# Performance work log

Measured on AMD Instinct MI355X. Metric: run time of the kernel, lower is better.

## Reference

```python
import jax, jax.numpy as jnp
import numpy as np

N_SENS, N_HID, N_MOT = 10000, 400000, 1000
E_SH, E_HH, E_HM = 4_000_000, 16_000_000, 400_000
BETA, THR, SLOPE = 0.9, 1.0, 25.0  # snn.Leaky(beta, threshold), surrogate.fast_sigmoid(slope=25)

# Heaviside spike with fast-sigmoid surrogate gradient (matches snnTorch)
@jax.custom_vjp
def spike(x):
    return (x > 0).astype(x.dtype)

def _spike_fwd(x):
    return (x > 0).astype(x.dtype), x

def _spike_bwd(x, g):
    return (g / (SLOPE * jnp.abs(x) + 1.0) ** 2,)

spike.defvjp(_spike_fwd, _spike_bwd)

def lif(inp, mem):
    # snn.Leaky, reset_mechanism='zero': mem = beta*mem + I; spike; reset to 0 where spiked
    mem = BETA * mem + inp
    spk = spike(mem - THR)
    mem = mem - jax.lax.stop_gradient(spk) * mem  # reset detached, as in snnTorch
    return spk, mem

def spmm_t(pre_idx, post_idx, w, pre_spikes, n_post):
    # torch.sparse.mm(W^T, pre_spikes): gather pre activity along edges, scatter-add to post
    contrib = w * pre_spikes[pre_idx]          # [E]
    return jax.ops.segment_sum(contrib, post_idx, num_segments=n_post)

def setup_inputs() -> dict:
    key = jax.random.key(0)
    ks = jax.random.split(key, 16)
    std_sh = 1.0 / np.sqrt(N_SENS * 0.001)
    std_hh = 1.0 / np.sqrt(N_HID * 0.0001)
    std_hm = 1.0 / np.sqrt(N_HID * 0.001)
    return {
        "sensory_input": jax.random.uniform(ks[0], (N_SENS,), jnp.float32),
        "sensory_mem": jax.random.uniform(ks[1], (N_SENS,), jnp.float32),
        "hidden_mem": jax.random.uniform(ks[2], (N_HID,), jnp.float32),
        "motor_mem": jax.random.uniform(ks[3], (N_MOT,), jnp.float32),
        "hidden_prev_spikes": (jax.random.uniform(ks[4], (N_HID,)) < 0.05).astype(jnp.float32),
        "w_sh": jax.random.normal(ks[5], (E_SH,), jnp.float32) * std_sh,
        "w_hh": jax.random.normal(ks[6], (E_HH,), jnp.float32) * std_hh,
        "w_hm": jax.random.normal(ks[7], (E_HM,), jnp.float32) * std_hm,
        "sh_pre": jax.random.randint(ks[8], (E_SH,), 0, N_SENS, jnp.int32),
        "sh_post": jax.random.randint(ks[9], (E_SH,), 0, N_HID, jnp.int32),
        "hh_pre": jax.random.randint(ks[10], (E_HH,), 0, N_HID, jnp.int32),
        "hh_post": jax.random.randint(ks[11], (E_HH,), 0, N_HID, jnp.int32),
        "hm_pre": jax.random.randint(ks[12], (E_HM,), 0, N_HID, jnp.int32),
        "hm_post": jax.random.randint(ks[13], (E_HM,), 0, N_MOT, jnp.int32),
    }

def reference(sensory_input, sensory_mem, hidden_mem, motor_mem, hidden_prev_spikes,
              w_sh, w_hh, w_hm, sh_pre, sh_post, hh_pre, hh_post, hm_pre, hm_post):
    sens_spk, _ = lif(sensory_input * 5.0, sensory_mem)
    hid_in = spmm_t(sh_pre, sh_post, w_sh, sens_spk, N_HID)
    hid_in = hid_in + 0.5 * spmm_t(hh_pre, hh_post, w_hh, hidden_prev_spikes, N_HID)
    hid_spk, _ = lif(hid_in * 5.0, hidden_mem)
    mot_in = spmm_t(hm_pre, hm_post, w_hm, hid_spk, N_MOT)
    mot_spk, _ = lif(mot_in * 20.0, motor_mem)
    return mot_spk
```

## Files before the change

kernel.cpp:

```cpp
#include <hip/hip_runtime.h>


#define N_SENS 10000
#define N_HID  400000
#define N_MOT  1000

#define CHUNK_LOG 14
#define CHUNK     (1 << CHUNK_LOG)
#define NBUCKET   25
#define CAP       204800
#define NCOPY     10

#define SENS_MW   320
#define HID_MW    12512

#define BUF_SH    4096
#define BUF_HH    2048
#define EPT_SH    4
#define EPT_HH    16

#define NB_HM     64

__global__ void make_masks(const float* __restrict__ sens_in,
                           const float* __restrict__ sens_mem,
                           const float* __restrict__ hid_prev,
                           uint2* __restrict__ smask,
                           uint2* __restrict__ hmask, int nb_sens) {
    bool pred = false;
    int i;
    uint2* dst;
    int maxw;
    if ((int)blockIdx.x < nb_sens) {
        i = blockIdx.x * blockDim.x + threadIdx.x;
        if (i < N_SENS) pred = (0.9f * sens_mem[i] + 5.0f * sens_in[i]) > 1.0f;
        dst = smask; maxw = SENS_MW / 2;
    } else {
        i = (blockIdx.x - nb_sens) * blockDim.x + threadIdx.x;
        if (i < N_HID) pred = (hid_prev[i] != 0.0f);
        dst = hmask; maxw = HID_MW / 2;
    }
    unsigned long long b = __ballot(pred);
    if ((threadIdx.x & 63) == 0) {
        int w = i >> 6;
        if (w < maxw) dst[w] = make_uint2((unsigned)b, (unsigned)(b >> 32));
    }
}

template <int MW, int BUFCAP, int EPT>
__global__ __launch_bounds__(1024, 8)
void bin_onepass(const int* __restrict__ pre, const int* __restrict__ post,
                 const float* __restrict__ w, const unsigned* __restrict__ gmask,
                 int n_e, float scale,
                 uint2* __restrict__ pairs, int* __restrict__ gcursor,
                 float* __restrict__ extra) {
    __shared__ unsigned sm[MW];
    __shared__ uint2 buf[BUFCAP];
    __shared__ int h[4][32];
    __shared__ int gb[32];
    __shared__ int lcur[32];
    __shared__ int total;

    const int tid = threadIdx.x;
    const int lane = tid & 63;
    for (int i = tid; i < MW; i += 1024) sm[i] = gmask[i];
    if (tid < 128) ((int*)h)[tid] = 0;
    if (tid == 0) total = 0;
    __syncthreads();

    int blockStart = blockIdx.x * (1024 * EPT);
    #pragma unroll
    for (int j = 0; j < EPT; ++j) {
        int e = blockStart + j * 1024 + tid;
        bool act = false;
        unsigned p = 0; float wv = 0.0f;
        if (e < n_e) {
            int pr = pre[e];
            act = (sm[pr >> 5] >> (pr & 31)) & 1u;
            if (act) { p = (unsigned)post[e]; wv = scale * w[e]; }
        }
        unsigned long long m = __ballot(act);
        if (m) {
            int rank = __popcll(m & ((1ull << lane) - 1ull));
            int base = 0;
            if (lane == 0) base = atomicAdd(&total, __popcll(m));
            base = __shfl(base, 0);
            if (act) {
                int k = base + rank;
                if (k < BUFCAP) buf[k] = make_uint2(p, __float_as_uint(wv));
                else atomicAdd(&extra[p], wv);
            }
        }
    }
    __syncthreads();
    int tot = total; if (tot > BUFCAP) tot = BUFCAP;

    int rep = (tid >> 6) & 3;
    for (int k = tid; k < tot; k += 1024)
        atomicAdd(&h[rep][buf[k].x >> CHUNK_LOG], 1);
    __syncthreads();
    if (tid < NBUCKET) {
        int hb = h[0][tid] + h[1][tid] + h[2][tid] + h[3][tid];
        gb[tid] = hb ? atomicAdd(&gcursor[tid], hb) : 0;
        lcur[tid] = 0;
    }
    __syncthreads();

    for (int k = tid; k < tot; k += 1024) {
        uint2 u = buf[k];
        int b = u.x >> CHUNK_LOG;
        int s = atomicAdd(&lcur[b], 1);
        int pos = gb[b] + s;
        if (pos < CAP)
            pairs[(size_t)b * CAP + pos] =
                make_uint2(u.x & (CHUNK - 1), u.y);
        else
            atomicAdd(&extra[u.x], __uint_as_float(u.y));
    }
}

__global__ __launch_bounds__(1024, 8)
void accum_bucket(const uint2* __restrict__ pairs,
                  const int* __restrict__ cursors,
                  float* __restrict__ partials) {
    int bucket = blockIdx.x / NCOPY;
    int copy   = blockIdx.x % NCOPY;
    __shared__ float acc[CHUNK];
    for (int i = threadIdx.x; i < CHUNK; i += blockDim.x) acc[i] = 0.0f;
    __syncthreads();

    int count = cursors[bucket];
    if (count > CAP) count = CAP;
    int begin = (int)((long long)count * copy / NCOPY);
    int end   = (int)((long long)count * (copy + 1) / NCOPY);
    const uint2* src = pairs + (size_t)bucket * CAP;
    for (int i = begin + threadIdx.x; i < end; i += blockDim.x) {
        uint2 u = src[i];
        atomicAdd(&acc[u.x], __uint_as_float(u.y));
    }
    __syncthreads();
    float* dst = partials + ((size_t)bucket * NCOPY + copy) * CHUNK;
    for (int i = threadIdx.x; i < CHUNK; i += blockDim.x) dst[i] = acc[i];
}

__global__ void reduce_lif_hidden_mask(const float* __restrict__ partials,
                                       const float* __restrict__ extra,
                                       const float* __restrict__ mem,
                                       uint2* __restrict__ mask) {
    int i = blockIdx.x * blockDim.x + threadIdx.x;
    bool pred = false;
    if (i < N_HID) {
        int b = i >> CHUNK_LOG, local = i & (CHUNK - 1);
        const float* p = partials + (size_t)b * NCOPY * CHUNK + local;
        float sum = extra[i];
        #pragma unroll
        for (int c = 0; c < NCOPY; ++c) sum += p[(size_t)c * CHUNK];
        pred = (0.9f * mem[i] + 5.0f * sum) > 1.0f;
    }
    unsigned long long bal = __ballot(pred);
    if ((threadIdx.x & 63) == 0) {
        int w = i >> 6;
        if (w < HID_MW / 2)
            mask[w] = make_uint2((unsigned)bal, (unsigned)(bal >> 32));
    }
}

__global__ __launch_bounds__(1024, 8)
void scatter_motor_mask(const int* __restrict__ pre,
                        const int* __restrict__ post,
                        const float* __restrict__ w,
                        const unsigned* __restrict__ gmask,
                        float* __restrict__ partials, int n_edges) {
    __shared__ float acc[N_MOT];
    __shared__ unsigned sm[HID_MW];
    for (int i = threadIdx.x; i < HID_MW; i += blockDim.x) sm[i] = gmask[i];
    for (int j = threadIdx.x; j < N_MOT; j += blockDim.x) acc[j] = 0.0f;
    __syncthreads();
    for (int e = blockIdx.x * blockDim.x + threadIdx.x; e < n_edges;
         e += gridDim.x * blockDim.x) {
        int pr = pre[e];
        if ((sm[pr >> 5] >> (pr & 31)) & 1u)
            atomicAdd(&acc[post[e]], w[e]);
    }
    __syncthreads();
    float* out = partials + (size_t)blockIdx.x * N_MOT;
    for (int j = threadIdx.x; j < N_MOT; j += blockDim.x) out[j] = acc[j];
}

__global__ void reduce_lif_motor(const float* __restrict__ partials, int nb,
                                 const float* __restrict__ mem,
                                 float* __restrict__ out) {
    int m = blockIdx.x * blockDim.x + threadIdx.x;
    if (m >= N_MOT) return;
    float sum = 0.0f;
    for (int b = 0; b < nb; ++b) sum += partials[(size_t)b * N_MOT + m];
    float v = 0.9f * mem[m] + 20.0f * sum;
    out[m] = (v > 1.0f) ? 1.0f : 0.0f;
}

__global__ void lif_kernel(const float* __restrict__ inp,
                           const float* __restrict__ mem_in,
                           float* __restrict__ spk,
                           float scale, int n) {
    int i = blockIdx.x * blockDim.x + threadIdx.x;
    if (i < n) {
        float m = 0.9f * mem_in[i] + scale * inp[i];
        spk[i] = (m > 1.0f) ? 1.0f : 0.0f;
    }
}

__global__ void scatter_dev(const int* __restrict__ pre,
                            const int* __restrict__ post,
                            const float* __restrict__ w,
                            const float* __restrict__ spikes,
                            float* __restrict__ out,
                            float scale, int n_edges) {
    int e = blockIdx.x * blockDim.x + threadIdx.x;
    if (e >= n_edges) return;
    float s = spikes[pre[e]];
    if (s != 0.0f) atomicAdd(&out[post[e]], scale * w[e] * s);
}

__global__ void lif_hidden_direct(const float* __restrict__ hid_in,
                                  const float* __restrict__ mem,
                                  float* __restrict__ spk) {
    int i = blockIdx.x * blockDim.x + threadIdx.x;
    if (i >= N_HID) return;
    float m = 0.9f * mem[i] + 5.0f * hid_in[i];
    spk[i] = (m > 1.0f) ? 1.0f : 0.0f;
}

__global__ void scatter_motor_f(const int* __restrict__ pre,
                                const int* __restrict__ post,
                                const float* __restrict__ w,
                                const float* __restrict__ spikes,
                                float* __restrict__ partials, int n_edges) {
    __shared__ float acc[N_MOT];
    for (int j = threadIdx.x; j < N_MOT; j += blockDim.x) acc[j] = 0.0f;
    __syncthreads();
    for (int e = blockIdx.x * blockDim.x + threadIdx.x; e < n_edges;
         e += gridDim.x * blockDim.x) {
        float s = spikes[pre[e]];
        if (s != 0.0f) atomicAdd(&acc[post[e]], w[e] * s);
    }
    __syncthreads();
    float* out = partials + (size_t)blockIdx.x * N_MOT;
    for (int j = threadIdx.x; j < N_MOT; j += blockDim.x) out[j] = acc[j];
}

extern "C" void kernel_launch(void* const* d_in, const int* in_sizes, int n_in,
                              void* d_out, int out_size, void* d_ws, size_t ws_size,
                              hipStream_t stream) {
    const float* sensory_input = (const float*)d_in[0];
    const float* sensory_mem   = (const float*)d_in[1];
    const float* hidden_mem    = (const float*)d_in[2];
    const float* motor_mem     = (const float*)d_in[3];
    const float* hidden_prev   = (const float*)d_in[4];
    const float* w_sh          = (const float*)d_in[5];
    const float* w_hh          = (const float*)d_in[6];
    const float* w_hm          = (const float*)d_in[7];
    const int*   sh_pre        = (const int*)d_in[8];
    const int*   sh_post       = (const int*)d_in[9];
    const int*   hh_pre        = (const int*)d_in[10];
    const int*   hh_post       = (const int*)d_in[11];
    const int*   hm_pre        = (const int*)d_in[12];
    const int*   hm_post       = (const int*)d_in[13];
    const int e_sh = in_sizes[5];
    const int e_hh = in_sizes[6];
    const int e_hm = in_sizes[7];
    const int B = 256;

    size_t o_cursor = 0;
    size_t o_extra  = 32;
    size_t o_pairs  = o_extra + N_HID;
    size_t o_part   = o_pairs + (size_t)NBUCKET * CAP * 2;
    size_t o_smask  = o_part + (size_t)NBUCKET * NCOPY * CHUNK;
    size_t o_hmaskp = o_smask + SENS_MW;
    size_t o_hmasks = o_hmaskp + HID_MW;
    size_t o_mpart  = o_hmasks + HID_MW;
    size_t f_need   = o_mpart + (size_t)NB_HM * N_MOT;
    bool fast = (ws_size / sizeof(float)) >= f_need;

    float* ws = (float*)d_ws;
    if (fast) {
        int*      cursors = (int*)(ws + o_cursor);
        float*    extra   = ws + o_extra;
        uint2*    pairs   = (uint2*)(ws + o_pairs);
        float*    part    = ws + o_part;
        unsigned* smask   = (unsigned*)(ws + o_smask);
        unsigned* hmaskp  = (unsigned*)(ws + o_hmaskp);
        unsigned* hmasks  = (unsigned*)(ws + o_hmasks);
        float*    mpart   = ws + o_mpart;

        hipMemsetAsync(cursors, 0, (32 + N_HID) * sizeof(float), stream);

        int nb_sens = (N_SENS + B - 1) / B;
        int nb_hidm = (N_HID + B - 1) / B;
        make_masks<<<nb_sens + nb_hidm, B, 0, stream>>>(
            sensory_input, sensory_mem, hidden_prev,
            (uint2*)smask, (uint2*)hmaskp, nb_sens);

        int nb_sh = (e_sh + 1024 * EPT_SH - 1) / (1024 * EPT_SH);
        int nb_hh = (e_hh + 1024 * EPT_HH - 1) / (1024 * EPT_HH);
        bin_onepass<SENS_MW, BUF_SH, EPT_SH><<<nb_sh, 1024, 0, stream>>>(
            sh_pre, sh_post, w_sh, smask, e_sh, 1.0f, pairs, cursors, extra);
        bin_onepass<HID_MW, BUF_HH, EPT_HH><<<nb_hh, 1024, 0, stream>>>(
            hh_pre, hh_post, w_hh, hmaskp, e_hh, 0.5f, pairs, cursors, extra);

        accum_bucket<<<NBUCKET * NCOPY, 1024, 0, stream>>>(pairs, cursors, part);
        reduce_lif_hidden_mask<<<(N_HID + B - 1) / B, B, 0, stream>>>(
            part, extra, hidden_mem, (uint2*)hmasks);
        scatter_motor_mask<<<NB_HM, 1024, 0, stream>>>(
            hm_pre, hm_post, w_hm, hmasks, mpart, e_hm);
        reduce_lif_motor<<<(N_MOT + B - 1) / B, B, 0, stream>>>(
            mpart, NB_HM, motor_mem, (float*)d_out);
    } else {
        float* hid_in   = ws;
        float* sens_spk = hid_in + N_HID;
        float* hid_spk  = sens_spk + 10016;
        float* mpart    = hid_spk + N_HID;
        hipMemsetAsync(hid_in, 0, (size_t)N_HID * sizeof(float), stream);
        lif_kernel<<<(N_SENS + B - 1) / B, B, 0, stream>>>(
            sensory_input, sensory_mem, sens_spk, 5.0f, N_SENS);
        scatter_dev<<<(e_sh + B - 1) / B, B, 0, stream>>>(
            sh_pre, sh_post, w_sh, sens_spk, hid_in, 1.0f, e_sh);
        scatter_dev<<<(e_hh + B - 1) / B, B, 0, stream>>>(
            hh_pre, hh_post, w_hh, hidden_prev, hid_in, 0.5f, e_hh);
        lif_hidden_direct<<<(N_HID + B - 1) / B, B, 0, stream>>>(
            hid_in, hidden_mem, hid_spk);
        scatter_motor_f<<<NB_HM, B, 0, stream>>>(
            hm_pre, hm_post, w_hm, hid_spk, mpart, e_hm);
        reduce_lif_motor<<<(N_MOT + B - 1) / B, B, 0, stream>>>(
            mpart, NB_HM, motor_mem, (float*)d_out);
    }
}
```

Baseline: 347.8 us.

## Batch edge loads in binning, fold memset into mask kernel, retune sizes

The binning kernel now loads all pre indices up front, tests the masks, then loads post and weight for active edges before the ballot and compaction step. This exposes more memory-level parallelism. The memset of cursors and the extra array is folded into make_masks, which removes one launch. Several sizes are retuned: NCOPY doubles, CAP shrinks, EPT_HH halves, and the motor scatter uses 128 blocks of 512 threads. The motor kernel no longer stages the hidden mask in shared memory and reads it from global memory instead, and the mask load is vectorised to uint4.

```diff
diff --git a/kernel.cpp b/kernel.cpp
--- a/kernel.cpp
+++ b/kernel.cpp
@@ -8,8 +8,8 @@
 #define CHUNK_LOG 14
 #define CHUNK     (1 << CHUNK_LOG)
 #define NBUCKET   25
-#define CAP       204800
-#define NCOPY     10
+#define CAP       196608
+#define NCOPY     20
 
 #define SENS_MW   320
 #define HID_MW    12512
@@ -17,26 +17,29 @@
 #define BUF_SH    4096
 #define BUF_HH    2048
 #define EPT_SH    4
-#define EPT_HH    16
-
-#define NB_HM     64
+#define EPT_HH    8
+
+#define NB_HM     128
 
 __global__ void make_masks(const float* __restrict__ sens_in,
                            const float* __restrict__ sens_mem,
                            const float* __restrict__ hid_prev,
                            uint2* __restrict__ smask,
-                           uint2* __restrict__ hmask, int nb_sens) {
+                           uint2* __restrict__ hmask,
+                           float* __restrict__ extra,
+                           int* __restrict__ cursors, int nb_sens) {
     bool pred = false;
     int i;
     uint2* dst;
     int maxw;
     if ((int)blockIdx.x < nb_sens) {
+        if (blockIdx.x == 0 && threadIdx.x < 32) cursors[threadIdx.x] = 0;
         i = blockIdx.x * blockDim.x + threadIdx.x;
         if (i < N_SENS) pred = (0.9f * sens_mem[i] + 5.0f * sens_in[i]) > 1.0f;
         dst = smask; maxw = SENS_MW / 2;
     } else {
         i = (blockIdx.x - nb_sens) * blockDim.x + threadIdx.x;
-        if (i < N_HID) pred = (hid_prev[i] != 0.0f);
+        if (i < N_HID) { pred = (hid_prev[i] != 0.0f); extra[i] = 0.0f; }
         dst = hmask; maxw = HID_MW / 2;
     }
     unsigned long long b = __ballot(pred);
@@ -48,11 +51,11 @@
 
 template <int MW, int BUFCAP, int EPT>
 __global__ __launch_bounds__(1024, 8)
-void bin_onepass(const int* __restrict__ pre, const int* __restrict__ post,
-                 const float* __restrict__ w, const unsigned* __restrict__ gmask,
-                 int n_e, float scale,
-                 uint2* __restrict__ pairs, int* __restrict__ gcursor,
-                 float* __restrict__ extra) {
+void bin_gather(const int* __restrict__ pre, const int* __restrict__ post,
+                const float* __restrict__ w, const unsigned* __restrict__ gmask,
+                int n_e, float scale,
+                uint2* __restrict__ pairs, int* __restrict__ gcursor,
+                float* __restrict__ extra) {
     __shared__ unsigned sm[MW];
     __shared__ uint2 buf[BUFCAP];
     __shared__ int h[4][32];
@@ -62,33 +65,46 @@
 
     const int tid = threadIdx.x;
     const int lane = tid & 63;
-    for (int i = tid; i < MW; i += 1024) sm[i] = gmask[i];
+    for (int i = tid; i < MW / 4; i += 1024)
+        ((uint4*)sm)[i] = ((const uint4*)gmask)[i];
     if (tid < 128) ((int*)h)[tid] = 0;
     if (tid == 0) total = 0;
     __syncthreads();
 
-    int blockStart = blockIdx.x * (1024 * EPT);
+    const int base = blockIdx.x * (1024 * EPT) + tid;
+
+    int pr[EPT];
     #pragma unroll
     for (int j = 0; j < EPT; ++j) {
-        int e = blockStart + j * 1024 + tid;
-        bool act = false;
-        unsigned p = 0; float wv = 0.0f;
-        if (e < n_e) {
-            int pr = pre[e];
-            act = (sm[pr >> 5] >> (pr & 31)) & 1u;
-            if (act) { p = (unsigned)post[e]; wv = scale * w[e]; }
+        int e = base + j * 1024;
+        pr[j] = (e < n_e) ? pre[e] : -1;
+    }
+    bool act[EPT];
+    #pragma unroll
+    for (int j = 0; j < EPT; ++j)
+        act[j] = (pr[j] >= 0) && ((sm[pr[j] >> 5] >> (pr[j] & 31)) & 1u);
+    unsigned p[EPT]; float wv[EPT];
+    #pragma unroll
+    for (int j = 0; j < EPT; ++j) {
+        p[j] = 0; wv[j] = 0.0f;
+        if (act[j]) {
+            int e = base + j * 1024;
+            p[j] = (unsigned)post[e];
+            wv[j] = scale * w[e];
         }
-        unsigned long long m = __ballot(act);
-        if (m) {
-            int rank = __popcll(m & ((1ull << lane) - 1ull));
-            int base = 0;
-            if (lane == 0) base = atomicAdd(&total, __popcll(m));
-            base = __shfl(base, 0);
-            if (act) {
-                int k = base + rank;
-                if (k < BUFCAP) buf[k] = make_uint2(p, __float_as_uint(wv));
-                else atomicAdd(&extra[p], wv);
-            }
+    }
+    #pragma unroll
+    for (int j = 0; j < EPT; ++j) {
+        unsigned long long m = __ballot(act[j]);
+        if (!m) continue;
+        int rank = __popcll(m & ((1ull << lane) - 1ull));
+        int bse = 0;
+        if (lane == 0) bse = atomicAdd(&total, __popcll(m));
+        bse = __shfl(bse, 0);
+        if (act[j]) {
+            int k = bse + rank;
+            if (k < BUFCAP) buf[k] = make_uint2(p[j], __float_as_uint(wv[j]));
+            else atomicAdd(&extra[p[j]], wv[j]);
         }
     }
     __syncthreads();
@@ -164,21 +180,19 @@
     }
 }
 
-__global__ __launch_bounds__(1024, 8)
+__global__ __launch_bounds__(512, 8)
 void scatter_motor_mask(const int* __restrict__ pre,
                         const int* __restrict__ post,
                         const float* __restrict__ w,
                         const unsigned* __restrict__ gmask,
                         float* __restrict__ partials, int n_edges) {
     __shared__ float acc[N_MOT];
-    __shared__ unsigned sm[HID_MW];
-    for (int i = threadIdx.x; i < HID_MW; i += blockDim.x) sm[i] = gmask[i];
     for (int j = threadIdx.x; j < N_MOT; j += blockDim.x) acc[j] = 0.0f;
     __syncthreads();
     for (int e = blockIdx.x * blockDim.x + threadIdx.x; e < n_edges;
          e += gridDim.x * blockDim.x) {
         int pr = pre[e];
-        if ((sm[pr >> 5] >> (pr & 31)) & 1u)
+        if ((gmask[pr >> 5] >> (pr & 31)) & 1u)
             atomicAdd(&acc[post[e]], w[e]);
     }
     __syncthreads();
@@ -291,25 +305,23 @@
         unsigned* hmasks  = (unsigned*)(ws + o_hmasks);
         float*    mpart   = ws + o_mpart;
 
-        hipMemsetAsync(cursors, 0, (32 + N_HID) * sizeof(float), stream);
-
         int nb_sens = (N_SENS + B - 1) / B;
         int nb_hidm = (N_HID + B - 1) / B;
         make_masks<<<nb_sens + nb_hidm, B, 0, stream>>>(
             sensory_input, sensory_mem, hidden_prev,
-            (uint2*)smask, (uint2*)hmaskp, nb_sens);
+            (uint2*)smask, (uint2*)hmaskp, extra, cursors, nb_sens);
 
         int nb_sh = (e_sh + 1024 * EPT_SH - 1) / (1024 * EPT_SH);
         int nb_hh = (e_hh + 1024 * EPT_HH - 1) / (1024 * EPT_HH);
-        bin_onepass<SENS_MW, BUF_SH, EPT_SH><<<nb_sh, 1024, 0, stream>>>(
+        bin_gather<SENS_MW, BUF_SH, EPT_SH><<<nb_sh, 1024, 0, stream>>>(
             sh_pre, sh_post, w_sh, smask, e_sh, 1.0f, pairs, cursors, extra);
-        bin_onepass<HID_MW, BUF_HH, EPT_HH><<<nb_hh, 1024, 0, stream>>>(
+        bin_gather<HID_MW, BUF_HH, EPT_HH><<<nb_hh, 1024, 0, stream>>>(
             hh_pre, hh_post, w_hh, hmaskp, e_hh, 0.5f, pairs, cursors, extra);
 
         accum_bucket<<<NBUCKET * NCOPY, 1024, 0, stream>>>(pairs, cursors, part);
         reduce_lif_hidden_mask<<<(N_HID + B - 1) / B, B, 0, stream>>>(
             part, extra, hidden_mem, (uint2*)hmasks);
-        scatter_motor_mask<<<NB_HM, 1024, 0, stream>>>(
+        scatter_motor_mask<<<NB_HM, 512, 0, stream>>>(
             hm_pre, hm_post, w_hm, hmasks, mpart, e_hm);
         reduce_lif_motor<<<(N_MOT + B - 1) / B, B, 0, stream>>>(
             mpart, NB_HM, motor_mem, (float*)d_out);
```

Result: slower. 356.4 us (+2.5%).
